# Kernel tuning notes

Hardware: AMD Instinct MI355X
Metric: run time of the kernel (lower is better)

Reference implementation:

```python
import jax, jax.numpy as jnp
import numpy as np

B, N, DIM = 64, 197, 768
NUM_HEAD, HEAD_DIM = 12, 64
SCALE = HEAD_DIM ** -0.5
WS = (14, 14)
NUM_REL = (2 * WS[0] - 1) * (2 * WS[1] - 1) + 3  # 732


def _relative_position_index():
    coords = np.stack(np.meshgrid(np.arange(WS[0]), np.arange(WS[1]), indexing='ij'))  # (2, Wh, Ww)
    cf = coords.reshape(2, -1)                              # (2, Wh*Ww)
    rel = (cf[:, :, None] - cf[:, None, :]).transpose(1, 2, 0).astype(np.int64)
    rel[:, :, 0] += WS[0] - 1
    rel[:, :, 1] += WS[1] - 1
    rel[:, :, 0] *= 2 * WS[1] - 1
    idx = np.zeros((WS[0] * WS[1] + 1,) * 2, dtype=np.int32)
    idx[1:, 1:] = rel.sum(-1)
    idx[0, :] = NUM_REL - 3
    idx[:, 0] = NUM_REL - 2
    idx[0, 0] = NUM_REL - 1
    return idx


def setup_inputs() -> dict:
    key = jax.random.key(0)
    k1, k2, k3, k4 = jax.random.split(key, 4)
    x = jax.random.normal(k1, (B, N, DIM), dtype=jnp.float32)
    qkv_w = jax.random.normal(k2, (3 * DIM, DIM), dtype=jnp.float32) * (DIM ** -0.5)
    q_bias = jnp.zeros((DIM,), dtype=jnp.float32)
    v_bias = jnp.zeros((DIM,), dtype=jnp.float32)
    rpb_table = jax.random.normal(k3, (NUM_REL, NUM_HEAD), dtype=jnp.float32) * 0.02
    proj_w = jax.random.normal(k4, (DIM, DIM), dtype=jnp.float32) * (DIM ** -0.5)
    proj_b = jnp.zeros((DIM,), dtype=jnp.float32)
    rel_index = jnp.asarray(_relative_position_index())
    return {"x": x, "qkv_w": qkv_w, "q_bias": q_bias, "v_bias": v_bias,
            "rpb_table": rpb_table, "proj_w": proj_w, "proj_b": proj_b,
            "rel_index": rel_index}


def reference(x, qkv_w, q_bias, v_bias, rpb_table, proj_w, proj_b, rel_index):
    b, n, c = x.shape
    # qkv projection with [q_bias, 0, v_bias] bias layout
    qkv_bias = jnp.concatenate([q_bias, jnp.zeros_like(v_bias), v_bias])
    qkv = x @ qkv_w.T + qkv_bias                               # (B, N, 3*C)
    qkv = qkv.reshape(b, n, 3, NUM_HEAD, HEAD_DIM).transpose(2, 0, 3, 1, 4)
    q, k, v = qkv[0] * SCALE, qkv[1], qkv[2]                   # (B, H, N, hd)
    attn = jnp.einsum('bhqd,bhkd->bhqk', q, k)                 # (B, H, N, N)
    # relative position bias gather: table[(N,N)] -> (N, N, H) -> (H, N, N)
    bias = rpb_table[rel_index].transpose(2, 0, 1)
    attn = jax.nn.softmax(attn + bias[None], axis=-1)
    out = jnp.einsum('bhqk,bhkd->bhqd', attn, v)               # (B, H, N, hd)
    out = out.transpose(0, 2, 1, 3).reshape(b, n, -1)
    return out @ proj_w.T + proj_b
```

## Files before the change

### kernel.cpp

```cpp
#include <hip/hip_runtime.h>


#define B_    64
#define N_    197
#define DIM_  768
#define H_    12
#define HD_   64
#define M_TOT (B_ * N_)

#define ST_A0   0
#define ST_A1   13312
#define ST_B0   26624
#define ST_B1   38912
#define OFF_Q   0
#define OFF_K   13312
#define OFF_VT  26624
#define LDS_TOT 51200

typedef __attribute__((ext_vector_type(8))) short bf8;
typedef __attribute__((ext_vector_type(4))) float f4;

__device__ __forceinline__ unsigned short f2bf(float f) {
    unsigned u = __float_as_uint(f);
    u = (u + 0x7fffu + ((u >> 16) & 1u)) >> 16;
    return (unsigned short)u;
}

__device__ __forceinline__ void gl2lds16(const unsigned short* g, unsigned short* l) {
    __builtin_amdgcn_global_load_lds(
        (const __attribute__((address_space(1))) void*)g,
        (__attribute__((address_space(3))) void*)l, 16, 0, 0);
}

__device__ __forceinline__ int qkaddr(int row, int col) {
    return row * 64 + ((((col >> 3) ^ row) & 7) << 3) + (col & 7);
}
__device__ __forceinline__ int vtaddr(int d, int k) {
    int s = k >> 3;
    int s2 = (s < 24) ? ((s & 24) | ((s ^ d) & 7)) : (24 + ((s ^ d) & 3));
    return d * 224 + (s2 << 3) + (k & 7);
}

__global__ void k_prep(const float* __restrict__ x, const float* __restrict__ qkvw,
                       const float* __restrict__ projw, const float* __restrict__ rpb,
                       const int* __restrict__ relidx,
                       unsigned short* __restrict__ x_bf, unsigned short* __restrict__ qkvw_bf,
                       unsigned short* __restrict__ projw_bf, float* __restrict__ bias_hqk) {
    const int T = gridDim.x * blockDim.x;
    const int tid = blockIdx.x * blockDim.x + threadIdx.x;
    for (int i = tid; i < M_TOT * DIM_; i += T) x_bf[i] = f2bf(x[i]);
    for (int i = tid; i < 3 * DIM_ * DIM_; i += T) qkvw_bf[i] = f2bf(qkvw[i]);
    for (int i = tid; i < DIM_ * DIM_; i += T) projw_bf[i] = f2bf(projw[i]);
    for (int i = tid; i < H_ * N_ * N_; i += T) {
        int h = i / (N_ * N_), qk = i - h * (N_ * N_);
        bias_hqk[i] = rpb[relidx[qk] * H_ + h];
    }
}

__global__ __launch_bounds__(1024) void k_fused(const unsigned short* __restrict__ X,
                                                const unsigned short* __restrict__ Wqkv,
                                                const float* __restrict__ qb,
                                                const float* __restrict__ vbias,
                                                const float* __restrict__ bias_hqk,
                                                unsigned short* __restrict__ att_ws) {
    __shared__ unsigned short lds[LDS_TOT];

    const int t = threadIdx.x;
    const int w = t >> 6, lane = t & 63, ln = lane & 15, quad = lane >> 4;
    const int wm = w & 3, wn = w >> 2;
    const int srl = lane >> 3;
    const int src8 = (lane & 7) ^ srl;

    const int gid = blockIdx.x;
    const int local = gid >> 3;
    const int b = (gid & 7) * 8 + (local & 7);
    const int h = local >> 3;

    const unsigned short* xb = X + (size_t)b * 197 * 768;

    auto stage = [&](int kt, int aOfs, int bOfs) {
#pragma unroll
        for (int i = 0; i < 4; ++i) {
            int idx = w + 16 * i;
            if (idx >= 50) break;
            if (idx < 26) {
                int tok = 8 * idx + srl;
                if (tok > 196) tok = 196;
                gl2lds16(xb + (size_t)tok * 768 + kt * 64 + src8 * 8,
                         &lds[aOfs + idx * 512]);
            } else {
                int bb = idx - 26;
                int rr = 8 * bb + srl;
                gl2lds16(Wqkv + (size_t)((rr >> 6) * 768 + h * 64 + (rr & 63)) * 768
                              + kt * 64 + src8 * 8,
                         &lds[bOfs + bb * 512]);
            }
        }
    };

    f4 acc[4][3] = {};

    auto compute = [&](int aOfs, int bOfs) {
#pragma unroll
        for (int ks = 0; ks < 2; ++ks) {
            bf8 bfr[3];
#pragma unroll
            for (int tl = 0; tl < 3; ++tl) {
                int rr = (wn * 3 + tl) * 16 + ln;
                int slot = (ks * 4 + quad) ^ (rr & 7);
                bfr[tl] = *(const bf8*)&lds[bOfs + rr * 64 + slot * 8];
            }
#pragma unroll
            for (int mi = 0; mi < 4; ++mi) {
                int mt = wm + 4 * mi;
                if (mt >= 13) continue;
                int row = mt * 16 + ln;
                int slot = (ks * 4 + quad) ^ (row & 7);
                bf8 af = *(const bf8*)&lds[aOfs + row * 64 + slot * 8];
#pragma unroll
                for (int tl = 0; tl < 3; ++tl)
                    acc[mi][tl] = __builtin_amdgcn_mfma_f32_16x16x32_bf16(
                        af, bfr[tl], acc[mi][tl], 0, 0, 0);
            }
        }
    };

    stage(0, ST_A0, ST_B0);
    for (int kt2 = 0; kt2 < 12; kt2 += 2) {
        __syncthreads();
        if (kt2 + 1 < 12) stage(kt2 + 1, ST_A1, ST_B1);
        compute(ST_A0, ST_B0);
        __syncthreads();
        if (kt2 + 2 < 12) stage(kt2 + 2, ST_A0, ST_B0);
        if (kt2 + 1 < 12) compute(ST_A1, ST_B1);
    }
    __syncthreads();

#pragma unroll
    for (int tl = 0; tl < 3; ++tl) {
        int tn = wn * 3 + tl;
        int p = tn >> 2;
        int col = (tn & 3) * 16 + ln;
        int d = h * 64 + col;
        float bj = (p == 0) ? qb[d] : (p == 2) ? vbias[d] : 0.0f;
#pragma unroll
        for (int mi = 0; mi < 4; ++mi) {
            int mt = wm + 4 * mi;
            if (mt >= 13) continue;
#pragma unroll
            for (int r = 0; r < 4; ++r) {
                int row = mt * 16 + quad * 4 + r;
                float v = acc[mi][tl][r];
                if (p == 0)      lds[OFF_Q + qkaddr(row, col)] = f2bf((v + bj) * 0.125f);
                else if (p == 1) lds[OFF_K + qkaddr(row, col)] = f2bf(v);
                else             lds[OFF_VT + vtaddr(col, row)] = f2bf(v + bj);
            }
        }
    }
    for (int idx = t; idx < 64 * 16; idx += 1024) {
        int d = idx >> 4, k = 208 + (idx & 15);
        lds[OFF_VT + vtaddr(d, k)] = 0;
    }
    __syncthreads();

    const float* bp = bias_hqk + (size_t)h * 197 * 197;

    for (int mt = w; mt < 13; mt += 16) {
        bf8 qa[2];
#pragma unroll
        for (int ks = 0; ks < 2; ++ks)
            qa[ks] = *(const bf8*)&lds[OFF_Q + qkaddr(mt * 16 + ln, ks * 32 + quad * 8)];

        f4 sacc[13];
#pragma unroll
        for (int nt = 0; nt < 13; ++nt) sacc[nt] = (f4){0.f, 0.f, 0.f, 0.f};
        __builtin_amdgcn_s_setprio(1);
#pragma unroll
        for (int nt = 0; nt < 13; ++nt) {
#pragma unroll
            for (int ks = 0; ks < 2; ++ks) {
                bf8 ka = *(const bf8*)&lds[OFF_K + qkaddr(nt * 16 + ln, ks * 32 + quad * 8)];
                sacc[nt] = __builtin_amdgcn_mfma_f32_16x16x32_bf16(ka, qa[ks], sacc[nt], 0, 0, 0);
            }
        }
        __builtin_amdgcn_s_setprio(0);

        int qg = mt * 16 + ln;
        const float* brow = bp + (size_t)(qg < 197 ? qg : 196) * 197;
        float mx = -3.0e38f;
#pragma unroll
        for (int nt = 0; nt < 13; ++nt)
#pragma unroll
            for (int r = 0; r < 4; ++r) {
                int kg = nt * 16 + quad * 4 + r;
                float s = (kg < 197) ? (sacc[nt][r] + brow[kg]) : -3.0e38f;
                sacc[nt][r] = s;
                mx = fmaxf(mx, s);
            }
        mx = fmaxf(mx, __shfl_xor(mx, 16, 64));
        mx = fmaxf(mx, __shfl_xor(mx, 32, 64));
        float sum = 0.f;
#pragma unroll
        for (int nt = 0; nt < 13; ++nt)
#pragma unroll
            for (int r = 0; r < 4; ++r) {
                float pv = __expf(sacc[nt][r] - mx);
                sacc[nt][r] = pv;
                sum += pv;
            }
        sum += __shfl_xor(sum, 16, 64);
        sum += __shfl_xor(sum, 32, 64);
        float inv = 1.0f / sum;

        unsigned pk[14][2];
#pragma unroll
        for (int nt = 0; nt < 13; ++nt) {
            pk[nt][0] = (unsigned)f2bf(sacc[nt][0] * inv) |
                        ((unsigned)f2bf(sacc[nt][1] * inv) << 16);
            pk[nt][1] = (unsigned)f2bf(sacc[nt][2] * inv) |
                        ((unsigned)f2bf(sacc[nt][3] * inv) << 16);
        }
        pk[13][0] = 0; pk[13][1] = 0;

        const int sA = (((lane & 15) | ((lane & 16) << 1)) << 2);
        const int sB = sA + 64;
        const bool hi = (lane & 32) != 0;
        f4 o[4];
#pragma unroll
        for (int j = 0; j < 4; ++j) o[j] = (f4){0.f, 0.f, 0.f, 0.f};
#pragma unroll
        for (int ks = 0; ks < 7; ++ks) {
            int b0 = __builtin_amdgcn_ds_bpermute(sA, (int)pk[2 * ks][0]);
            int b1 = __builtin_amdgcn_ds_bpermute(sA, (int)pk[2 * ks][1]);
            int b2 = __builtin_amdgcn_ds_bpermute(sB, (int)pk[2 * ks][0]);
            int b3 = __builtin_amdgcn_ds_bpermute(sB, (int)pk[2 * ks][1]);
            int c0 = __builtin_amdgcn_ds_bpermute(sA, (int)pk[2 * ks + 1][0]);
            int c1 = __builtin_amdgcn_ds_bpermute(sA, (int)pk[2 * ks + 1][1]);
            int c2 = __builtin_amdgcn_ds_bpermute(sB, (int)pk[2 * ks + 1][0]);
            int c3 = __builtin_amdgcn_ds_bpermute(sB, (int)pk[2 * ks + 1][1]);
            union { int u[4]; bf8 v; } uu;
            uu.u[0] = hi ? c0 : b0;
            uu.u[1] = hi ? c1 : b1;
            uu.u[2] = hi ? c2 : b2;
            uu.u[3] = hi ? c3 : b3;
            __builtin_amdgcn_s_setprio(1);
#pragma unroll
            for (int j = 0; j < 4; ++j) {
                bf8 vf = *(const bf8*)&lds[OFF_VT + vtaddr(j * 16 + ln, ks * 32 + quad * 8)];
                o[j] = __builtin_amdgcn_mfma_f32_16x16x32_bf16(uu.v, vf, o[j], 0, 0, 0);
            }
            __builtin_amdgcn_s_setprio(0);
        }
#pragma unroll
        for (int j = 0; j < 4; ++j)
#pragma unroll
            for (int r = 0; r < 4; ++r) {
                int tok = mt * 16 + quad * 4 + r;
                if (tok < 197)
                    att_ws[((size_t)b * 197 + tok) * 768 + h * 64 + j * 16 + ln] = f2bf(o[j][r]);
            }
    }
}

__device__ __forceinline__ void pj_stage(const unsigned short* __restrict__ A,
                                         const unsigned short* __restrict__ Bm,
                                         int bm, int bn, int kt, int w, int rsub, int src8,
                                         unsigned short* a_l, unsigned short* b_l) {
#pragma unroll
    for (int c = 0; c < 4; ++c) {
        int rb = w * 32 + c * 8;
        int gr = bm * 128 + rb + rsub;
        if (gr > M_TOT - 1) gr = M_TOT - 1;
        gl2lds16(A + (size_t)gr * 768 + kt * 64 + (src8 << 3), &a_l[rb * 64]);
        int gc = bn * 128 + rb + rsub;
        gl2lds16(Bm + (size_t)gc * 768 + kt * 64 + (src8 << 3), &b_l[rb * 64]);
    }
}

__device__ __forceinline__ void pj_compute(const unsigned short* a_l, const unsigned short* b_l,
                                           int wm, int wn, int ln, int quad, f4 (*acc)[4]) {
#pragma unroll
    for (int ks = 0; ks < 2; ++ks) {
        bf8 af[4], bfr[4];
#pragma unroll
        for (int i = 0; i < 4; ++i)
            af[i] = *(const bf8*)&a_l[((wm * 64 + i * 16 + ln) << 6) +
                                      ((((ks << 2) + quad) ^ (ln & 7)) << 3)];
#pragma unroll
        for (int j = 0; j < 4; ++j)
            bfr[j] = *(const bf8*)&b_l[((wn * 64 + j * 16 + ln) << 6) +
                                       ((((ks << 2) + quad) ^ (ln & 7)) << 3)];
#pragma unroll
        for (int i = 0; i < 4; ++i)
#pragma unroll
            for (int j = 0; j < 4; ++j)
                acc[i][j] = __builtin_amdgcn_mfma_f32_16x16x32_bf16(af[i], bfr[j], acc[i][j], 0, 0, 0);
    }
}

__global__ __launch_bounds__(256) void k_proj(const unsigned short* __restrict__ A,
                                              const unsigned short* __restrict__ Bm,
                                              const float* __restrict__ pb,
                                              float* __restrict__ out) {
    __shared__ unsigned short a0[128 * 64], a1[128 * 64];
    __shared__ unsigned short b0[128 * 64], b1[128 * 64];
    const int t = threadIdx.x;
    const int w = t >> 6, lane = t & 63, ln = lane & 15, quad = lane >> 4;
    const int wm = w & 1, wn = w >> 1;

    const int gid = blockIdx.x;
    const int panel = gid / 48, rem = gid - panel * 48;
    const int pm0 = panel * 8;
    const int psz = (99 - pm0 < 8) ? (99 - pm0) : 8;
    const int bm = pm0 + rem % psz;
    const int bn = rem / psz;

    const int rsub = lane >> 3;
    const int src8 = (lane & 7) ^ rsub;

    f4 acc[4][4] = {};

    pj_stage(A, Bm, bm, bn, 0, w, rsub, src8, a0, b0);
#pragma unroll
    for (int kt2 = 0; kt2 < 12; kt2 += 2) {
        __syncthreads();
        if (kt2 + 1 < 12) pj_stage(A, Bm, bm, bn, kt2 + 1, w, rsub, src8, a1, b1);
        pj_compute(a0, b0, wm, wn, ln, quad, acc);
        __syncthreads();
        if (kt2 + 2 < 12) pj_stage(A, Bm, bm, bn, kt2 + 2, w, rsub, src8, a0, b0);
        if (kt2 + 1 < 12) pj_compute(a1, b1, wm, wn, ln, quad, acc);
    }

#pragma unroll
    for (int i = 0; i < 4; ++i) {
#pragma unroll
        for (int r = 0; r < 4; ++r) {
            int row_g = bm * 128 + wm * 64 + i * 16 + quad * 4 + r;
            if (row_g >= M_TOT) continue;
#pragma unroll
            for (int j = 0; j < 4; ++j) {
                int col_g = bn * 128 + wn * 64 + j * 16 + ln;
                out[(size_t)row_g * 768 + col_g] = acc[i][j][r] + pb[col_g];
            }
        }
    }
}

extern "C" void kernel_launch(void* const* d_in, const int* in_sizes, int n_in,
                              void* d_out, int out_size, void* d_ws, size_t ws_size,
                              hipStream_t stream) {
    const float* x     = (const float*)d_in[0];
    const float* qkvw  = (const float*)d_in[1];
    const float* qb    = (const float*)d_in[2];
    const float* vb    = (const float*)d_in[3];
    const float* rpb   = (const float*)d_in[4];
    const float* projw = (const float*)d_in[5];
    const float* pb    = (const float*)d_in[6];
    const int*   ridx  = (const int*)d_in[7];
    float* out = (float*)d_out;

    char* ws = (char*)d_ws;
    size_t off = 0;
    auto alloc = [&](size_t bytes) -> void* {
        void* p = ws + off;
        off = (off + bytes + 255) & ~(size_t)255;
        return p;
    };
    unsigned short* x_bf     = (unsigned short*)alloc((size_t)M_TOT * DIM_ * 2);
    unsigned short* qkvw_bf  = (unsigned short*)alloc((size_t)3 * DIM_ * DIM_ * 2);
    unsigned short* projw_bf = (unsigned short*)alloc((size_t)DIM_ * DIM_ * 2);
    float*          bias_h   = (float*)alloc((size_t)H_ * N_ * N_ * 4);
    unsigned short* att_ws   = (unsigned short*)alloc((size_t)(M_TOT + 64) * DIM_ * 2);
    (void)ws_size; (void)in_sizes; (void)n_in; (void)out_size;

    k_prep<<<1200, 256, 0, stream>>>(x, qkvw, projw, rpb, ridx,
                                     x_bf, qkvw_bf, projw_bf, bias_h);
    k_fused<<<768, 1024, 0, stream>>>(x_bf, qkvw_bf, qb, vb, bias_h, att_ws);
    k_proj<<<594, 256, 0, stream>>>(att_ws, projw_bf, pb, out);
}
```

Measured before the change: 222.3 us.

## Triple-buffer QKV GEMM loads and use explicit vmcnt waits with single barrier

The QKV projection GEMM moves from two LDS stage buffers to three, prefetching two k-tiles ahead. Each iteration waits with s_waitcnt vmcnt(3) so only the oldest tile's global-to-LDS loads must finish, then takes one raw s_barrier instead of two __syncthreads. The output projection GEMM keeps double buffering but also switches to a single explicit vmcnt(0) plus s_barrier per k-step. The goal is more overlap of global loads with MFMA work and fewer barriers, at the cost of more LDS (76.8KB), which may lower occupancy, and reliance on the vmcnt count matching the number of loads issued per stage.

```diff
diff --git a/kernel.cpp b/kernel.cpp
--- a/kernel.cpp
+++ b/kernel.cpp
@@ -10,12 +10,14 @@
 
 #define ST_A0   0
 #define ST_A1   13312
-#define ST_B0   26624
-#define ST_B1   38912
+#define ST_A2   26624
+#define ST_B0   39936
+#define ST_B1   52224
+#define ST_B2   64512
 #define OFF_Q   0
 #define OFF_K   13312
 #define OFF_VT  26624
-#define LDS_TOT 51200
+#define LDS_TOT 76800
 
 typedef __attribute__((ext_vector_type(8))) short bf8;
 typedef __attribute__((ext_vector_type(4))) float f4;
@@ -125,14 +127,19 @@
         }
     };
 
+    const int stA[3] = {ST_A0, ST_A1, ST_A2};
+    const int stB[3] = {ST_B0, ST_B1, ST_B2};
     stage(0, ST_A0, ST_B0);
-    for (int kt2 = 0; kt2 < 12; kt2 += 2) {
-        __syncthreads();
-        if (kt2 + 1 < 12) stage(kt2 + 1, ST_A1, ST_B1);
-        compute(ST_A0, ST_B0);
-        __syncthreads();
-        if (kt2 + 2 < 12) stage(kt2 + 2, ST_A0, ST_B0);
-        if (kt2 + 1 < 12) compute(ST_A1, ST_B1);
+    stage(1, ST_A1, ST_B1);
+#pragma unroll
+    for (int kt = 0; kt < 12; ++kt) {
+        if (kt < 11) { __asm__ __volatile__("s_waitcnt vmcnt(3)" ::: "memory"); }
+        else         { __asm__ __volatile__("s_waitcnt vmcnt(0)" ::: "memory"); }
+        __builtin_amdgcn_sched_barrier(0);
+        __builtin_amdgcn_s_barrier();
+        __builtin_amdgcn_sched_barrier(0);
+        if (kt + 2 < 12) stage(kt + 2, stA[(kt + 2) % 3], stB[(kt + 2) % 3]);
+        compute(stA[kt % 3], stB[kt % 3]);
     }
     __syncthreads();
 
@@ -322,13 +329,14 @@
 
     pj_stage(A, Bm, bm, bn, 0, w, rsub, src8, a0, b0);
 #pragma unroll
-    for (int kt2 = 0; kt2 < 12; kt2 += 2) {
-        __syncthreads();
-        if (kt2 + 1 < 12) pj_stage(A, Bm, bm, bn, kt2 + 1, w, rsub, src8, a1, b1);
-        pj_compute(a0, b0, wm, wn, ln, quad, acc);
-        __syncthreads();
-        if (kt2 + 2 < 12) pj_stage(A, Bm, bm, bn, kt2 + 2, w, rsub, src8, a0, b0);
-        if (kt2 + 1 < 12) pj_compute(a1, b1, wm, wn, ln, quad, acc);
+    for (int kt = 0; kt < 12; ++kt) {
+        __asm__ __volatile__("s_waitcnt vmcnt(0)" ::: "memory");
+        __builtin_amdgcn_sched_barrier(0);
+        __builtin_amdgcn_s_barrier();
+        __builtin_amdgcn_sched_barrier(0);
+        if (kt + 1 < 12) pj_stage(A, Bm, bm, bn, kt + 1, w, rsub, src8,
+                                  (kt & 1) ? a0 : a1, (kt & 1) ? b0 : b1);
+        pj_compute((kt & 1) ? a1 : a0, (kt & 1) ? b1 : b0, wm, wn, ln, quad, acc);
     }
 
 #pragma unroll
```

Result: no change. 220.1 us (-1.0%).
